# Performance work log

Measured on AMD Instinct MI355X. Metric: run time of the kernel, lower is better.

The kernel has to match this reference:

```python
import jax, jax.numpy as jnp
import numpy as np

NUM_NODES = 100000
EMBED_DIM = 64
NUM_LAYERS = 3
NUM_EDGES = 1250000


def setup_inputs() -> dict:
    key = jax.random.key(0)
    k1, k2 = jax.random.split(key)
    edge_index = jax.random.randint(k1, (2, NUM_EDGES), 0, NUM_NODES, dtype=jnp.int64)
    # xavier_uniform for Embedding weight: bound = sqrt(6/(fan_in+fan_out))
    bound = float(np.sqrt(6.0 / (NUM_NODES + EMBED_DIM)))
    emb = jax.random.uniform(k2, (NUM_NODES, EMBED_DIM), dtype=jnp.float32,
                             minval=-bound, maxval=bound)
    return {"edge_index": edge_index, "emb": emb}


def reference(edge_index, emb):
    row, col = edge_index[0], edge_index[1]
    num_nodes = emb.shape[0]
    # degree from source index (bincount over row)
    deg = jax.ops.segment_sum(jnp.ones_like(row, dtype=emb.dtype), row,
                              num_segments=num_nodes)
    deg_inv_sqrt = jnp.where(deg > 0, jax.lax.rsqrt(jnp.maximum(deg, 1.0)) * jnp.where(deg > 0, 1.0, 0.0), 0.0)
    deg_inv_sqrt = jnp.where(deg > 0, deg ** -0.5, 0.0)

    x = emb
    acc = emb  # running sum of all_embeddings
    for _ in range(NUM_LAYERS):
        m = deg_inv_sqrt[row][:, None] * x[col]           # [E, D] gather + scale
        x = jax.ops.segment_sum(m, row, num_segments=num_nodes)  # scatter-add
        x = x * deg_inv_sqrt[:, None]
        acc = acc + x
    return acc / (NUM_LAYERS + 1)
```

## Files before the change

### kernel.cpp

```cpp
#include <hip/hip_runtime.h>
#include <math.h>

#define N_NODES 100000
#define DIM 64
#define N_EDGES 1250000
#define SCAN_BLOCKS 256
#define RPB 128
#define NB_BUCKETS ((N_NODES + RPB - 1) / RPB)
#define NBLK_B 128
#define CNT_N (NB_BUCKETS * NBLK_B)
#define CAP 2048

typedef unsigned short ushort_t;
typedef unsigned int uint_t;
typedef _Float16 h2 __attribute__((ext_vector_type(2)));

__device__ __forceinline__ float hlo(uint_t u) {
    return (float)__builtin_bit_cast(_Float16, (ushort_t)(u & 0xFFFFu));
}
__device__ __forceinline__ float hhi(uint_t u) {
    return (float)__builtin_bit_cast(_Float16, (ushort_t)(u >> 16));
}
__device__ __forceinline__ uint_t f2h(float f) {
    return (uint_t)__builtin_bit_cast(ushort_t, (_Float16)f);
}

__device__ __forceinline__ void dacc(float& a0, float& a1, uint_t u) {
#if __has_builtin(__builtin_amdgcn_fdot2)
    h2 h = __builtin_bit_cast(h2, u);
    const h2 e0 = {(_Float16)1.0f, (_Float16)0.0f};
    const h2 e1 = {(_Float16)0.0f, (_Float16)1.0f};
    a0 = __builtin_amdgcn_fdot2(h, e0, a0, false);
    a1 = __builtin_amdgcn_fdot2(h, e1, a1, false);
#else
    a0 += hlo(u);
    a1 += hhi(u);
#endif
}

__device__ __forceinline__ void dacc4(float* acc, uint4 v) {
    dacc(acc[0], acc[1], v.x); dacc(acc[2], acc[3], v.y);
    dacc(acc[4], acc[5], v.z); dacc(acc[6], acc[7], v.w);
}

__global__ void conv_hist_kernel(const float* __restrict__ emb, ushort_t* __restrict__ embh,
                                 int n8, const int* __restrict__ row,
                                 int* __restrict__ cnt, int E) {
    __shared__ int h[NB_BUCKETS];
    if (blockIdx.x < NBLK_B) {
        for (int i = threadIdx.x; i < NB_BUCKETS; i += blockDim.x) h[i] = 0;
        __syncthreads();
        int blk = blockIdx.x;
        int per = (E + NBLK_B - 1) / NBLK_B;
        int lo = blk * per, hi = min(lo + per, E);
        for (int e = lo + (int)threadIdx.x; e < hi; e += blockDim.x)
            atomicAdd(&h[row[e] >> 7], 1);
        __syncthreads();
        for (int b = threadIdx.x; b < NB_BUCKETS; b += blockDim.x)
            cnt[b * NBLK_B + blk] = h[b];
    } else {
        int i = (blockIdx.x - NBLK_B) * blockDim.x + threadIdx.x;
        if (i < n8) {
            float4 a = reinterpret_cast<const float4*>(emb)[2 * i];
            float4 b = reinterpret_cast<const float4*>(emb)[2 * i + 1];
            uint4 w;
            w.x = f2h(a.x) | (f2h(a.y) << 16);
            w.y = f2h(a.z) | (f2h(a.w) << 16);
            w.z = f2h(b.x) | (f2h(b.y) << 16);
            w.w = f2h(b.z) | (f2h(b.w) << 16);
            reinterpret_cast<uint4*>(embh)[i] = w;
        }
    }
}

__global__ void partial_kernel(const int* __restrict__ in, int* __restrict__ blocksum,
                               int N, int chunk) {
    __shared__ int sh[256];
    int b = blockIdx.x;
    int lo = b * chunk, hi = min(lo + chunk, N);
    int s = 0;
    for (int i = lo + (int)threadIdx.x; i < hi; i += 256) s += in[i];
    sh[threadIdx.x] = s;
    __syncthreads();
    for (int off = 128; off > 0; off >>= 1) {
        if ((int)threadIdx.x < off) sh[threadIdx.x] += sh[threadIdx.x + off];
        __syncthreads();
    }
    if (threadIdx.x == 0) blocksum[b] = sh[0];
}

__global__ void scan_small_kernel(int* __restrict__ blocksum, int* __restrict__ out, int N) {
    __shared__ int sh[SCAN_BLOCKS];
    int t = threadIdx.x;
    int v = blocksum[t];
    sh[t] = v;
    __syncthreads();
    for (int off = 1; off < SCAN_BLOCKS; off <<= 1) {
        int u = (t >= off) ? sh[t - off] : 0;
        __syncthreads();
        sh[t] += u;
        __syncthreads();
    }
    blocksum[t] = sh[t] - v;
    if (t == SCAN_BLOCKS - 1) out[N] = sh[SCAN_BLOCKS - 1];
}

__global__ void scan_emit_kernel(const int* __restrict__ in, const int* __restrict__ blocksum,
                                 int* __restrict__ out, int N, int chunk) {
    __shared__ int sh[256];
    int b = blockIdx.x;
    int t = threadIdx.x;
    int lo = b * chunk, hi = min(lo + chunk, N);
    int running = blocksum[b];
    for (int base = lo; base < hi; base += 256) {
        int i = base + t;
        int d = (i < hi) ? in[i] : 0;
        sh[t] = d;
        __syncthreads();
        for (int off = 1; off < 256; off <<= 1) {
            int u = (t >= off) ? sh[t - off] : 0;
            __syncthreads();
            sh[t] += u;
            __syncthreads();
        }
        if (i < hi) out[i] = running + (sh[t] - d);
        running += sh[255];
        __syncthreads();
    }
}

__global__ void bucket_scatter_kernel(const int* __restrict__ row, const int* __restrict__ col,
                                      const int* __restrict__ slot_off,
                                      int* __restrict__ pairs, int E) {
    __shared__ int cur[NB_BUCKETS];
    int blk = blockIdx.x;
    for (int b = threadIdx.x; b < NB_BUCKETS; b += blockDim.x)
        cur[b] = slot_off[b * NBLK_B + blk];
    __syncthreads();
    int per = (E + (int)gridDim.x - 1) / (int)gridDim.x;
    int lo = blk * per, hi = min(lo + per, E);
    for (int e = lo + (int)threadIdx.x; e < hi; e += blockDim.x) {
        int r = row[e], c = col[e];
        int pos = atomicAdd(&cur[r >> 7], 1);
        pairs[pos] = ((r & (RPB - 1)) << 17) | c;
    }
}

__global__ void __launch_bounds__(256) bucket_csr_kernel(
        const int* __restrict__ slot_off, const int* __restrict__ pairs,
        int* __restrict__ row_ptr, float* __restrict__ dis,
        int* __restrict__ csr_col, int E) {
    __shared__ int pk[CAP];
    __shared__ int csr_lds[CAP];
    __shared__ int deg_loc[RPB];
    __shared__ int scan_loc[RPB];
    __shared__ int cur_loc[RPB];
    int b = blockIdx.x;
    int t = threadIdx.x;
    int start = slot_off[b * NBLK_B];
    int end = slot_off[(b + 1) * NBLK_B];
    int cnt = end - start;
    bool fits = (cnt <= CAP);

    if (t < RPB) deg_loc[t] = 0;
    if (fits) {
        for (int i = t; i < cnt; i += 256) pk[i] = pairs[start + i];
    }
    __syncthreads();
    for (int i = t; i < cnt; i += 256) {
        int p = fits ? pk[i] : pairs[start + i];
        atomicAdd(&deg_loc[p >> 17], 1);
    }
    __syncthreads();
    int d = (t < RPB) ? deg_loc[t] : 0;
    if (t < RPB) scan_loc[t] = d;
    __syncthreads();
    for (int off = 1; off < RPB; off <<= 1) {
        int v = (t < RPB && t >= off) ? scan_loc[t - off] : 0;
        __syncthreads();
        if (t < RPB) scan_loc[t] += v;
        __syncthreads();
    }
    if (t < RPB) {
        int exc = scan_loc[t] - d;
        cur_loc[t] = exc;
        int rg = b * RPB + t;
        if (rg < N_NODES) {
            row_ptr[rg] = start + exc;
            dis[rg] = (d > 0) ? (float)(1.0 / sqrt((double)d)) : 0.0f;
        }
    }
    __syncthreads();
    for (int i = t; i < cnt; i += 256) {
        int p = fits ? pk[i] : pairs[start + i];
        int pos = atomicAdd(&cur_loc[p >> 17], 1);
        int c = (p & 0x1FFFF) << 7;
        if (fits) csr_lds[pos] = c;
        else      csr_col[start + pos] = c;
    }
    __syncthreads();
    if (fits) {
        for (int i = t; i < cnt; i += 256) csr_col[start + i] = csr_lds[i];
    }
    if (b == NB_BUCKETS - 1 && t == 0) row_ptr[N_NODES] = E;
}

template <int MODE>
__global__ void gather_kernel(const int* __restrict__ row_ptr, const int* __restrict__ csr_col,
                              const float* __restrict__ dis,
                              const ushort_t* __restrict__ x_old, ushort_t* __restrict__ x_new,
                              const ushort_t* __restrict__ e0, const ushort_t* __restrict__ x1,
                              const ushort_t* __restrict__ x2, float* __restrict__ out,
                              int Npair) {
    int lane = threadIdx.x & 63;
    int sub = lane >> 5;
    int l5 = lane & 31;
    int g = l5 >> 3;
    int l = l5 & 7;
    int lb = l * 16;
    const char* xb = (const char*)x_old;

    int wave0 = (int)((blockIdx.x * (size_t)blockDim.x + threadIdx.x) >> 6);
    int nwaves = (int)(((size_t)gridDim.x * blockDim.x) >> 6);

    for (int wid = wave0; wid < Npair; wid += nwaves) {
        int node = wid * 2 + sub;
        int start = row_ptr[node];
        int end = row_ptr[node + 1];

        float acc[8];
        #pragma unroll
        for (int k = 0; k < 8; ++k) acc[k] = 0.f;

        int e = start + g;
        if (e < end) {
            int o0 = csr_col[e];
            int o1 = (e + 4 < end) ? csr_col[e + 4] : 0;
            while (e + 4 < end) {
                uint4 v0 = *reinterpret_cast<const uint4*>(xb + o0 + lb);
                uint4 v1 = *reinterpret_cast<const uint4*>(xb + o1 + lb);
                o0 = csr_col[min(e + 8, N_EDGES - 1)];
                o1 = csr_col[min(e + 12, N_EDGES - 1)];
                dacc4(acc, v0); dacc4(acc, v1);
                e += 8;
            }
            if (e < end) {
                uint4 v0 = *reinterpret_cast<const uint4*>(xb + o0 + lb);
                dacc4(acc, v0);
            }
        }

        #pragma unroll
        for (int off = 8; off <= 16; off <<= 1) {
            #pragma unroll
            for (int k = 0; k < 8; ++k) acc[k] += __shfl_xor(acc[k], off, 64);
        }

        if (g == 0) {
            float s = dis[node];
            float s2 = s * s;
            if (MODE != 2) {
                uint4 w;
                w.x = f2h(acc[0] * s2) | (f2h(acc[1] * s2) << 16);
                w.y = f2h(acc[2] * s2) | (f2h(acc[3] * s2) << 16);
                w.z = f2h(acc[4] * s2) | (f2h(acc[5] * s2) << 16);
                w.w = f2h(acc[6] * s2) | (f2h(acc[7] * s2) << 16);
                *reinterpret_cast<uint4*>(&x_new[(size_t)node * DIM + l * 8]) = w;
            } else {
                size_t ob = (size_t)node * (DIM * 2) + lb;
                uint4 ea  = *reinterpret_cast<const uint4*>((const char*)e0 + ob);
                uint4 u1  = *reinterpret_cast<const uint4*>((const char*)x1 + ob);
                uint4 u2  = *reinterpret_cast<const uint4*>((const char*)x2 + ob);
                float4 r0, r1;
                r0.x = (hlo(ea.x) + hlo(u1.x) + hlo(u2.x) + acc[0] * s2) * 0.25f;
                r0.y = (hhi(ea.x) + hhi(u1.x) + hhi(u2.x) + acc[1] * s2) * 0.25f;
                r0.z = (hlo(ea.y) + hlo(u1.y) + hlo(u2.y) + acc[2] * s2) * 0.25f;
                r0.w = (hhi(ea.y) + hhi(u1.y) + hhi(u2.y) + acc[3] * s2) * 0.25f;
                r1.x = (hlo(ea.z) + hlo(u1.z) + hlo(u2.z) + acc[4] * s2) * 0.25f;
                r1.y = (hhi(ea.z) + hhi(u1.z) + hhi(u2.z) + acc[5] * s2) * 0.25f;
                r1.z = (hlo(ea.w) + hlo(u1.w) + hlo(u2.w) + acc[6] * s2) * 0.25f;
                r1.w = (hhi(ea.w) + hhi(u1.w) + hhi(u2.w) + acc[7] * s2) * 0.25f;
                size_t oo = (size_t)node * DIM + l * 8;
                *reinterpret_cast<float4*>(&out[oo]) = r0;
                *reinterpret_cast<float4*>(&out[oo + 4]) = r1;
            }
        }
    }
}

extern "C" void kernel_launch(void* const* d_in, const int* in_sizes, int n_in,
                              void* d_out, int out_size, void* d_ws, size_t ws_size,
                              hipStream_t stream) {
    const int* edge = (const int*)d_in[0];
    const int* row = edge;
    const int* col = edge + N_EDGES;
    const float* emb = (const float*)d_in[1];
    float* out = (float*)d_out;

    char* ws = (char*)d_ws;
    size_t off = 0;
    auto alloc = [&](size_t bytes) {
        char* p = ws + off;
        off += (bytes + 255) & ~(size_t)255;
        return p;
    };
    int*      row_ptr  = (int*)alloc(((size_t)N_NODES + 1) * sizeof(int));
    float*    dis      = (float*)alloc((size_t)N_NODES * sizeof(float));
    int*      blocksum = (int*)alloc((size_t)SCAN_BLOCKS * sizeof(int));
    int*      cnt      = (int*)alloc((size_t)CNT_N * sizeof(int));
    int*      slot_off = (int*)alloc(((size_t)CNT_N + 1) * sizeof(int));
    int*      csr_col  = (int*)alloc((size_t)N_EDGES * sizeof(int));
    ushort_t* embh     = (ushort_t*)alloc((size_t)N_NODES * DIM * sizeof(ushort_t));
    ushort_t* x1       = (ushort_t*)alloc((size_t)N_NODES * DIM * sizeof(ushort_t));
    ushort_t* x2       = (ushort_t*)alloc((size_t)N_NODES * DIM * sizeof(ushort_t));
    int*      pairs    = (int*)x2;

    const int gather_blocks = 2048;
    const int chunk = (CNT_N + SCAN_BLOCKS - 1) / SCAN_BLOCKS;
    const int n8 = N_NODES * DIM / 8;

    conv_hist_kernel<<<NBLK_B + (n8 + 255) / 256, 256, 0, stream>>>(emb, embh, n8, row, cnt, N_EDGES);
    partial_kernel<<<SCAN_BLOCKS, 256, 0, stream>>>(cnt, blocksum, CNT_N, chunk);
    scan_small_kernel<<<1, SCAN_BLOCKS, 0, stream>>>(blocksum, slot_off, CNT_N);
    scan_emit_kernel<<<SCAN_BLOCKS, 256, 0, stream>>>(cnt, blocksum, slot_off, CNT_N, chunk);
    bucket_scatter_kernel<<<NBLK_B, 256, 0, stream>>>(row, col, slot_off, pairs, N_EDGES);
    bucket_csr_kernel<<<NB_BUCKETS, 256, 0, stream>>>(slot_off, pairs, row_ptr, dis, csr_col, N_EDGES);

    gather_kernel<0><<<gather_blocks, 256, 0, stream>>>(row_ptr, csr_col, dis, embh, x1,
                                                        nullptr, nullptr, nullptr, nullptr, N_NODES / 2);
    gather_kernel<1><<<gather_blocks, 256, 0, stream>>>(row_ptr, csr_col, dis, x1, x2,
                                                        nullptr, nullptr, nullptr, nullptr, N_NODES / 2);
    gather_kernel<2><<<gather_blocks, 256, 0, stream>>>(row_ptr, csr_col, dis, x2, nullptr,
                                                        embh, x1, x2, out, N_NODES / 2);
}
```

Before: 133.8 us.

## Fuse CSR build stages into one cooperative kernel with grid syncs

Merges the histogram/fp16-convert, three scan kernels, bucket scatter and per-bucket CSR build into a single cooperative kernel of 512 blocks separated by grid.sync barriers. The aim is to remove five kernel launch gaps and their inter-kernel drain overhead. In exchange, the conversion and CSR stages now loop over work with fewer blocks, which lowers parallelism in the bucket stage. Grid-wide barriers also carry their own cost, and the single-block scan is now repeated redundantly in every scan block.

```diff
diff --git a/kernel.cpp b/kernel.cpp
--- a/kernel.cpp
+++ b/kernel.cpp
@@ -1,5 +1,8 @@
 #include <hip/hip_runtime.h>
+#include <hip/hip_cooperative_groups.h>
 #include <math.h>
+
+namespace cg = cooperative_groups;
 
 #define N_NODES 100000
 #define DIM 64
@@ -10,6 +13,7 @@
 #define NBLK_B 128
 #define CNT_N (NB_BUCKETS * NBLK_B)
 #define CAP 2048
+#define BGRID 512
 
 typedef unsigned short ushort_t;
 typedef unsigned int uint_t;
@@ -43,166 +47,161 @@
     dacc(acc[4], acc[5], v.z); dacc(acc[6], acc[7], v.w);
 }
 
-__global__ void conv_hist_kernel(const float* __restrict__ emb, ushort_t* __restrict__ embh,
-                                 int n8, const int* __restrict__ row,
-                                 int* __restrict__ cnt, int E) {
-    __shared__ int h[NB_BUCKETS];
-    if (blockIdx.x < NBLK_B) {
-        for (int i = threadIdx.x; i < NB_BUCKETS; i += blockDim.x) h[i] = 0;
-        __syncthreads();
-        int blk = blockIdx.x;
-        int per = (E + NBLK_B - 1) / NBLK_B;
-        int lo = blk * per, hi = min(lo + per, E);
-        for (int e = lo + (int)threadIdx.x; e < hi; e += blockDim.x)
-            atomicAdd(&h[row[e] >> 7], 1);
-        __syncthreads();
-        for (int b = threadIdx.x; b < NB_BUCKETS; b += blockDim.x)
-            cnt[b * NBLK_B + blk] = h[b];
+struct CsrShared { int pk[CAP]; int csr[CAP]; int deg[RPB]; int scn[RPB]; int cur[RPB]; };
+union BuildShared {
+    int h[NB_BUCKETS];
+    int sh[SCAN_BLOCKS];
+    CsrShared c;
+};
+
+__global__ void __launch_bounds__(256) build_kernel(
+        const float* __restrict__ emb, ushort_t* __restrict__ embh,
+        const int* __restrict__ row, const int* __restrict__ col,
+        int* __restrict__ cnt, int* __restrict__ blocksum,
+        int* __restrict__ slot_off, int* __restrict__ pairs,
+        int* __restrict__ row_ptr, float* __restrict__ dis,
+        int* __restrict__ csr_col) {
+    cg::grid_group grid = cg::this_grid();
+    __shared__ BuildShared S;
+    int t = threadIdx.x;
+    int blk = blockIdx.x;
+    const int n8 = N_NODES * DIM / 8;
+    const int chunk = (CNT_N + SCAN_BLOCKS - 1) / SCAN_BLOCKS;
+
+    if (blk < NBLK_B) {
+        for (int i = t; i < NB_BUCKETS; i += 256) S.h[i] = 0;
+        __syncthreads();
+        int per = (N_EDGES + NBLK_B - 1) / NBLK_B;
+        int lo = blk * per, hi = min(lo + per, N_EDGES);
+        for (int e = lo + t; e < hi; e += 256)
+            atomicAdd(&S.h[row[e] >> 7], 1);
+        __syncthreads();
+        for (int b = t; b < NB_BUCKETS; b += 256)
+            cnt[b * NBLK_B + blk] = S.h[b];
     } else {
-        int i = (blockIdx.x - NBLK_B) * blockDim.x + threadIdx.x;
-        if (i < n8) {
+        const int nconv = BGRID - NBLK_B;
+        for (int i = (blk - NBLK_B) * 256 + t; i < n8; i += nconv * 256) {
             float4 a = reinterpret_cast<const float4*>(emb)[2 * i];
-            float4 b = reinterpret_cast<const float4*>(emb)[2 * i + 1];
+            float4 b4 = reinterpret_cast<const float4*>(emb)[2 * i + 1];
             uint4 w;
             w.x = f2h(a.x) | (f2h(a.y) << 16);
             w.y = f2h(a.z) | (f2h(a.w) << 16);
-            w.z = f2h(b.x) | (f2h(b.y) << 16);
-            w.w = f2h(b.z) | (f2h(b.w) << 16);
+            w.z = f2h(b4.x) | (f2h(b4.y) << 16);
+            w.w = f2h(b4.z) | (f2h(b4.w) << 16);
             reinterpret_cast<uint4*>(embh)[i] = w;
         }
     }
-}
-
-__global__ void partial_kernel(const int* __restrict__ in, int* __restrict__ blocksum,
-                               int N, int chunk) {
-    __shared__ int sh[256];
-    int b = blockIdx.x;
-    int lo = b * chunk, hi = min(lo + chunk, N);
-    int s = 0;
-    for (int i = lo + (int)threadIdx.x; i < hi; i += 256) s += in[i];
-    sh[threadIdx.x] = s;
-    __syncthreads();
-    for (int off = 128; off > 0; off >>= 1) {
-        if ((int)threadIdx.x < off) sh[threadIdx.x] += sh[threadIdx.x + off];
-        __syncthreads();
-    }
-    if (threadIdx.x == 0) blocksum[b] = sh[0];
-}
-
-__global__ void scan_small_kernel(int* __restrict__ blocksum, int* __restrict__ out, int N) {
-    __shared__ int sh[SCAN_BLOCKS];
-    int t = threadIdx.x;
-    int v = blocksum[t];
-    sh[t] = v;
-    __syncthreads();
-    for (int off = 1; off < SCAN_BLOCKS; off <<= 1) {
-        int u = (t >= off) ? sh[t - off] : 0;
-        __syncthreads();
-        sh[t] += u;
-        __syncthreads();
-    }
-    blocksum[t] = sh[t] - v;
-    if (t == SCAN_BLOCKS - 1) out[N] = sh[SCAN_BLOCKS - 1];
-}
-
-__global__ void scan_emit_kernel(const int* __restrict__ in, const int* __restrict__ blocksum,
-                                 int* __restrict__ out, int N, int chunk) {
-    __shared__ int sh[256];
-    int b = blockIdx.x;
-    int t = threadIdx.x;
-    int lo = b * chunk, hi = min(lo + chunk, N);
-    int running = blocksum[b];
-    for (int base = lo; base < hi; base += 256) {
-        int i = base + t;
-        int d = (i < hi) ? in[i] : 0;
-        sh[t] = d;
-        __syncthreads();
-        for (int off = 1; off < 256; off <<= 1) {
-            int u = (t >= off) ? sh[t - off] : 0;
-            __syncthreads();
-            sh[t] += u;
-            __syncthreads();
-        }
-        if (i < hi) out[i] = running + (sh[t] - d);
-        running += sh[255];
-        __syncthreads();
-    }
-}
-
-__global__ void bucket_scatter_kernel(const int* __restrict__ row, const int* __restrict__ col,
-                                      const int* __restrict__ slot_off,
-                                      int* __restrict__ pairs, int E) {
-    __shared__ int cur[NB_BUCKETS];
-    int blk = blockIdx.x;
-    for (int b = threadIdx.x; b < NB_BUCKETS; b += blockDim.x)
-        cur[b] = slot_off[b * NBLK_B + blk];
-    __syncthreads();
-    int per = (E + (int)gridDim.x - 1) / (int)gridDim.x;
-    int lo = blk * per, hi = min(lo + per, E);
-    for (int e = lo + (int)threadIdx.x; e < hi; e += blockDim.x) {
-        int r = row[e], c = col[e];
-        int pos = atomicAdd(&cur[r >> 7], 1);
-        pairs[pos] = ((r & (RPB - 1)) << 17) | c;
-    }
-}
-
-__global__ void __launch_bounds__(256) bucket_csr_kernel(
-        const int* __restrict__ slot_off, const int* __restrict__ pairs,
-        int* __restrict__ row_ptr, float* __restrict__ dis,
-        int* __restrict__ csr_col, int E) {
-    __shared__ int pk[CAP];
-    __shared__ int csr_lds[CAP];
-    __shared__ int deg_loc[RPB];
-    __shared__ int scan_loc[RPB];
-    __shared__ int cur_loc[RPB];
-    int b = blockIdx.x;
-    int t = threadIdx.x;
-    int start = slot_off[b * NBLK_B];
-    int end = slot_off[(b + 1) * NBLK_B];
-    int cnt = end - start;
-    bool fits = (cnt <= CAP);
-
-    if (t < RPB) deg_loc[t] = 0;
-    if (fits) {
-        for (int i = t; i < cnt; i += 256) pk[i] = pairs[start + i];
-    }
-    __syncthreads();
-    for (int i = t; i < cnt; i += 256) {
-        int p = fits ? pk[i] : pairs[start + i];
-        atomicAdd(&deg_loc[p >> 17], 1);
-    }
-    __syncthreads();
-    int d = (t < RPB) ? deg_loc[t] : 0;
-    if (t < RPB) scan_loc[t] = d;
-    __syncthreads();
-    for (int off = 1; off < RPB; off <<= 1) {
-        int v = (t < RPB && t >= off) ? scan_loc[t - off] : 0;
-        __syncthreads();
-        if (t < RPB) scan_loc[t] += v;
-        __syncthreads();
-    }
-    if (t < RPB) {
-        int exc = scan_loc[t] - d;
-        cur_loc[t] = exc;
-        int rg = b * RPB + t;
-        if (rg < N_NODES) {
-            row_ptr[rg] = start + exc;
-            dis[rg] = (d > 0) ? (float)(1.0 / sqrt((double)d)) : 0.0f;
-        }
-    }
-    __syncthreads();
-    for (int i = t; i < cnt; i += 256) {
-        int p = fits ? pk[i] : pairs[start + i];
-        int pos = atomicAdd(&cur_loc[p >> 17], 1);
-        int c = (p & 0x1FFFF) << 7;
-        if (fits) csr_lds[pos] = c;
-        else      csr_col[start + pos] = c;
-    }
-    __syncthreads();
-    if (fits) {
-        for (int i = t; i < cnt; i += 256) csr_col[start + i] = csr_lds[i];
-    }
-    if (b == NB_BUCKETS - 1 && t == 0) row_ptr[N_NODES] = E;
+    grid.sync();
+
+    if (blk < SCAN_BLOCKS) {
+        int lo = blk * chunk, hi = min(lo + chunk, CNT_N);
+        int s = 0;
+        for (int i = lo + t; i < hi; i += 256) s += cnt[i];
+        S.sh[t] = s;
+        __syncthreads();
+        for (int off = 128; off > 0; off >>= 1) {
+            if (t < off) S.sh[t] += S.sh[t + off];
+            __syncthreads();
+        }
+        if (t == 0) blocksum[blk] = S.sh[0];
+    }
+    grid.sync();
+
+    if (blk < SCAN_BLOCKS) {
+        int v = blocksum[t];
+        S.sh[t] = v;
+        __syncthreads();
+        for (int off = 1; off < SCAN_BLOCKS; off <<= 1) {
+            int u = (t >= off) ? S.sh[t - off] : 0;
+            __syncthreads();
+            S.sh[t] += u;
+            __syncthreads();
+        }
+        int running = (blk > 0) ? S.sh[blk - 1] : 0;
+        int total = S.sh[SCAN_BLOCKS - 1];
+        __syncthreads();
+        int lo = blk * chunk, hi = min(lo + chunk, CNT_N);
+        for (int base = lo; base < hi; base += 256) {
+            int i = base + t;
+            int d = (i < hi) ? cnt[i] : 0;
+            S.sh[t] = d;
+            __syncthreads();
+            for (int off = 1; off < 256; off <<= 1) {
+                int u = (t >= off) ? S.sh[t - off] : 0;
+                __syncthreads();
+                S.sh[t] += u;
+                __syncthreads();
+            }
+            if (i < hi) slot_off[i] = running + (S.sh[t] - d);
+            running += S.sh[255];
+            __syncthreads();
+        }
+        if (blk == 0 && t == 0) slot_off[CNT_N] = total;
+    }
+    grid.sync();
+
+    if (blk < NBLK_B) {
+        for (int b = t; b < NB_BUCKETS; b += 256)
+            S.h[b] = slot_off[b * NBLK_B + blk];
+        __syncthreads();
+        int per = (N_EDGES + NBLK_B - 1) / NBLK_B;
+        int lo = blk * per, hi = min(lo + per, N_EDGES);
+        for (int e = lo + t; e < hi; e += 256) {
+            int r = row[e], c = col[e];
+            int pos = atomicAdd(&S.h[r >> 7], 1);
+            pairs[pos] = ((r & (RPB - 1)) << 17) | c;
+        }
+    }
+    grid.sync();
+
+    for (int b = blk; b < NB_BUCKETS; b += BGRID) {
+        int start = slot_off[b * NBLK_B];
+        int end = slot_off[(b + 1) * NBLK_B];
+        int cntb = end - start;
+        bool fits = (cntb <= CAP);
+        if (t < RPB) S.c.deg[t] = 0;
+        if (fits) {
+            for (int i = t; i < cntb; i += 256) S.c.pk[i] = pairs[start + i];
+        }
+        __syncthreads();
+        for (int i = t; i < cntb; i += 256) {
+            int p = fits ? S.c.pk[i] : pairs[start + i];
+            atomicAdd(&S.c.deg[p >> 17], 1);
+        }
+        __syncthreads();
+        int d = (t < RPB) ? S.c.deg[t] : 0;
+        if (t < RPB) S.c.scn[t] = d;
+        __syncthreads();
+        for (int off = 1; off < RPB; off <<= 1) {
+            int v2 = (t < RPB && t >= off) ? S.c.scn[t - off] : 0;
+            __syncthreads();
+            if (t < RPB) S.c.scn[t] += v2;
+            __syncthreads();
+        }
+        if (t < RPB) {
+            int exc = S.c.scn[t] - d;
+            S.c.cur[t] = exc;
+            int rg = b * RPB + t;
+            if (rg < N_NODES) {
+                row_ptr[rg] = start + exc;
+                dis[rg] = (d > 0) ? (float)(1.0 / sqrt((double)d)) : 0.0f;
+            }
+        }
+        __syncthreads();
+        for (int i = t; i < cntb; i += 256) {
+            int p = fits ? S.c.pk[i] : pairs[start + i];
+            int pos = atomicAdd(&S.c.cur[p >> 17], 1);
+            int c = (p & 0x1FFFF) << 7;
+            if (fits) S.c.csr[pos] = c;
+            else      csr_col[start + pos] = c;
+        }
+        __syncthreads();
+        if (fits) {
+            for (int i = t; i < cntb; i += 256) csr_col[start + i] = S.c.csr[i];
+        }
+        if (b == NB_BUCKETS - 1 && t == 0) row_ptr[N_NODES] = N_EDGES;
+        __syncthreads();
+    }
 }
 
 template <int MODE>
@@ -316,15 +315,12 @@
     int*      pairs    = (int*)x2;
 
     const int gather_blocks = 2048;
-    const int chunk = (CNT_N + SCAN_BLOCKS - 1) / SCAN_BLOCKS;
-    const int n8 = N_NODES * DIM / 8;
-
-    conv_hist_kernel<<<NBLK_B + (n8 + 255) / 256, 256, 0, stream>>>(emb, embh, n8, row, cnt, N_EDGES);
-    partial_kernel<<<SCAN_BLOCKS, 256, 0, stream>>>(cnt, blocksum, CNT_N, chunk);
-    scan_small_kernel<<<1, SCAN_BLOCKS, 0, stream>>>(blocksum, slot_off, CNT_N);
-    scan_emit_kernel<<<SCAN_BLOCKS, 256, 0, stream>>>(cnt, blocksum, slot_off, CNT_N, chunk);
-    bucket_scatter_kernel<<<NBLK_B, 256, 0, stream>>>(row, col, slot_off, pairs, N_EDGES);
-    bucket_csr_kernel<<<NB_BUCKETS, 256, 0, stream>>>(slot_off, pairs, row_ptr, dis, csr_col, N_EDGES);
+
+    void* args[] = {(void*)&emb, (void*)&embh, (void*)&row, (void*)&col,
+                    (void*)&cnt, (void*)&blocksum, (void*)&slot_off, (void*)&pairs,
+                    (void*)&row_ptr, (void*)&dis, (void*)&csr_col};
+    hipLaunchCooperativeKernel((void*)build_kernel, dim3(BGRID), dim3(256),
+                               args, 0, stream);
 
     gather_kernel<0><<<gather_blocks, 256, 0, stream>>>(row_ptr, csr_col, dis, embh, x1,
                                                         nullptr, nullptr, nullptr, nullptr, N_NODES / 2);
```

Measured after the change: 371.0 us. +177.3%, slower.
